# Optimization experiments

Measured on AMD Instinct MI355X. Metric: run time of the kernel, lower is better.

The kernel has to match this reference:

```python
import jax, jax.numpy as jnp
import numpy as np

N_NODES = 50000
N_EDGES = 800000
IN_CH = 128
HID = 128


def setup_inputs() -> dict:
    key = jax.random.key(0)
    ks = jax.random.split(key, 16)
    inp = {
        "x": jax.random.normal(ks[0], (N_NODES, IN_CH), dtype=jnp.float32),
        "edge_index": jax.random.randint(ks[1], (2, N_EDGES), 0, N_NODES, dtype=jnp.int64),
        "batch_size": 1024,
    }
    dims = [(IN_CH, HID), (HID, HID), (HID, HID)]
    for i, (din, dout) in enumerate(dims):
        s = 1.0 / np.sqrt(din)
        inp[f"W_l{i}"] = jax.random.uniform(ks[2 + 4 * i], (dout, din), jnp.float32, -s, s)
        inp[f"b_l{i}"] = jax.random.uniform(ks[3 + 4 * i], (dout,), jnp.float32, -s, s)
        inp[f"W_r{i}"] = jax.random.uniform(ks[4 + 4 * i], (dout, din), jnp.float32, -s, s)
        inp[f"a{i}"] = jnp.full((dout,), 0.25, dtype=jnp.float32)  # PReLU slope
    return inp


def _sage_prelu(x, src, dst, W_l, b_l, W_r, a):
    # mean aggregation of source messages at target nodes
    msg_sum = jax.ops.segment_sum(x[src], dst, num_segments=N_NODES)  # [N, din]
    deg = jax.ops.segment_sum(jnp.ones((src.shape[0],), x.dtype), dst, num_segments=N_NODES)
    agg = msg_sum / jnp.maximum(deg, 1.0)[:, None]
    out = agg @ W_l.T + b_l + x @ W_r.T  # lin_l(aggr) + lin_r(x), bias on lin_l only
    return jnp.where(out > 0, out, a * out)  # per-channel PReLU


def reference(x, edge_index, batch_size, W_l0, b_l0, W_r0, a0, W_l1, b_l1, W_r1, a1, W_l2, b_l2, W_r2, a2):
    src, dst = edge_index[0], edge_index[1]
    x = _sage_prelu(x, src, dst, W_l0, b_l0, W_r0, a0)
    x = _sage_prelu(x, src, dst, W_l1, b_l1, W_r1, a1)
    x = _sage_prelu(x, src, dst, W_l2, b_l2, W_r2, a2)
    return x[:batch_size]
```

## Files before the change

### kernel.cpp

```cpp
#include <hip/hip_runtime.h>

#define NN 50000
#define NE 800000
#define C 128
#define CAP 64
#define EP4 ((NE / 4 + 255) / 256)
#define SPLITB 1563
#define WB 96
#define CB  ((NN + 255) / 256)
#define AGG0B ((NN + 3) / 4)
#define ASTRIDE 136

typedef __attribute__((ext_vector_type(8))) short bf16x8;
typedef __attribute__((ext_vector_type(4))) float f32x4;
typedef unsigned short ushort;

__device__ inline ushort bf16_rn(float f) {
    unsigned u = __builtin_bit_cast(unsigned, f);
    u += 0x7FFF + ((u >> 16) & 1);
    return (ushort)(u >> 16);
}
__device__ inline void split_bf16(float f, ushort& hi, ushort& lo) {
    hi = bf16_rn(f);
    float hif = __builtin_bit_cast(float, (unsigned)hi << 16);
    lo = bf16_rn(f - hif);
}
__device__ inline float bf_lo(unsigned u) { return __builtin_bit_cast(float, u << 16); }
__device__ inline float bf_hi(unsigned u) { return __builtin_bit_cast(float, u & 0xFFFF0000u); }


__global__ __launch_bounds__(256)
void prep_kernel(const int* __restrict__ src, const int* __restrict__ dst,
                 const float* __restrict__ x,
                 const float* __restrict__ W0, const float* __restrict__ W1,
                 const float* __restrict__ W2, const float* __restrict__ W3,
                 const float* __restrict__ W4, const float* __restrict__ W5,
                 int* __restrict__ deg, int* __restrict__ col,
                 ushort* __restrict__ Ah,
                 ushort* __restrict__ Wh, ushort* __restrict__ Wl,
                 int* __restrict__ needed, int rows_out) {
    int t = threadIdx.x;
    if (blockIdx.x < EP4) {
        int e0 = (blockIdx.x * 256 + t) * 4;
        if (e0 < NE) {
            int4 da = *(const int4*)(dst + e0);
            int4 sa = *(const int4*)(src + e0);
            int p0 = atomicAdd(&deg[da.x], 1);
            int p1 = atomicAdd(&deg[da.y], 1);
            int p2 = atomicAdd(&deg[da.z], 1);
            int p3 = atomicAdd(&deg[da.w], 1);
            if (p0 < CAP) col[da.x * CAP + p0] = sa.x;
            if (p1 < CAP) col[da.y * CAP + p1] = sa.y;
            if (p2 < CAP) col[da.z * CAP + p2] = sa.z;
            if (p3 < CAP) col[da.w * CAP + p3] = sa.w;
            if (da.x < rows_out) needed[sa.x] = 1;
            if (da.y < rows_out) needed[sa.y] = 1;
            if (da.z < rows_out) needed[sa.z] = 1;
            if (da.w < rows_out) needed[sa.w] = 1;
        }
    } else if (blockIdx.x < EP4 + SPLITB) {
        int tid = (blockIdx.x - EP4) * 256 + t;
        const int total = NN * C / 4;
        for (int i = tid; i < total; i += SPLITB * 256) {
            f32x4 v = ((const f32x4*)x)[i];
            ushort h0 = bf16_rn(v.x), h1 = bf16_rn(v.y);
            ushort h2 = bf16_rn(v.z), h3 = bf16_rn(v.w);
            *(uint2*)(Ah + (size_t)i * 4) = make_uint2((unsigned)h0 | ((unsigned)h1 << 16),
                                                       (unsigned)h2 | ((unsigned)h3 << 16));
        }
    } else {
        const float* Ws[6] = {W0, W1, W2, W3, W4, W5};
        int i = (blockIdx.x - EP4 - SPLITB) * 256 + t;
        int mat = i >> 12;
        f32x4 v = ((const f32x4*)Ws[mat])[i & 4095];
        ushort h0, h1, h2, h3, l0, l1, l2, l3;
        split_bf16(v.x, h0, l0);
        split_bf16(v.y, h1, l1);
        split_bf16(v.z, h2, l2);
        split_bf16(v.w, h3, l3);
        *(uint2*)(Wh + (size_t)i * 4) = make_uint2((unsigned)h0 | ((unsigned)h1 << 16),
                                                   (unsigned)h2 | ((unsigned)h3 << 16));
        *(uint2*)(Wl + (size_t)i * 4) = make_uint2((unsigned)l0 | ((unsigned)l1 << 16),
                                                   (unsigned)l2 | ((unsigned)l3 << 16));
    }
}


__global__ __launch_bounds__(256)
void agg_kernel(const ushort* __restrict__ xh, const int* __restrict__ deg,
                const int* __restrict__ col,
                const int* __restrict__ list, const int* __restrict__ countp,
                ushort* __restrict__ aggh, ushort* __restrict__ aggl, int nodes,
                int aggblocks, const int* __restrict__ needed,
                int* __restrict__ wlist, int* __restrict__ wcnt, int rows_out) {
    if (needed && blockIdx.x >= aggblocks) {
        int i = (blockIdx.x - aggblocks) * 256 + threadIdx.x;
        if (i < NN && (i < rows_out || needed[i])) {
            int p = atomicAdd(wcnt, 1);
            wlist[p] = i;
        }
        return;
    }
    int i = (blockIdx.x * blockDim.x + threadIdx.x) >> 6;
    int lane = threadIdx.x & 63;
    int cnt = list ? *countp : nodes;
    if (i >= cnt) return;
    int node = list ? list[i] : i;
    int quad = lane >> 4;
    int ql   = lane & 15;
    int d = min(deg[node], CAP);
    int start = node * CAP;
    int end = start + d;
    const uint4* xr = (const uint4*)xh;
    float a0=0,a1=0,a2=0,a3=0,a4=0,a5=0,a6=0,a7=0;
    int e = start;
    for (; e + 15 < end; e += 16) {
        int i0 = col[e + quad];
        int i1 = col[e + 4 + quad];
        int i2 = col[e + 8 + quad];
        int i3 = col[e + 12 + quad];
        uint4 u0 = xr[(size_t)i0 * 16 + ql];
        uint4 u1 = xr[(size_t)i1 * 16 + ql];
        uint4 u2 = xr[(size_t)i2 * 16 + ql];
        uint4 u3 = xr[(size_t)i3 * 16 + ql];
        a0 += (bf_lo(u0.x) + bf_lo(u1.x)) + (bf_lo(u2.x) + bf_lo(u3.x));
        a1 += (bf_hi(u0.x) + bf_hi(u1.x)) + (bf_hi(u2.x) + bf_hi(u3.x));
        a2 += (bf_lo(u0.y) + bf_lo(u1.y)) + (bf_lo(u2.y) + bf_lo(u3.y));
        a3 += (bf_hi(u0.y) + bf_hi(u1.y)) + (bf_hi(u2.y) + bf_hi(u3.y));
        a4 += (bf_lo(u0.z) + bf_lo(u1.z)) + (bf_lo(u2.z) + bf_lo(u3.z));
        a5 += (bf_hi(u0.z) + bf_hi(u1.z)) + (bf_hi(u2.z) + bf_hi(u3.z));
        a6 += (bf_lo(u0.w) + bf_lo(u1.w)) + (bf_lo(u2.w) + bf_lo(u3.w));
        a7 += (bf_hi(u0.w) + bf_hi(u1.w)) + (bf_hi(u2.w) + bf_hi(u3.w));
    }
    for (; e + 7 < end; e += 8) {
        int i0 = col[e + quad];
        int i1 = col[e + 4 + quad];
        uint4 u0 = xr[(size_t)i0 * 16 + ql];
        uint4 u1 = xr[(size_t)i1 * 16 + ql];
        a0 += bf_lo(u0.x) + bf_lo(u1.x); a1 += bf_hi(u0.x) + bf_hi(u1.x);
        a2 += bf_lo(u0.y) + bf_lo(u1.y); a3 += bf_hi(u0.y) + bf_hi(u1.y);
        a4 += bf_lo(u0.z) + bf_lo(u1.z); a5 += bf_hi(u0.z) + bf_hi(u1.z);
        a6 += bf_lo(u0.w) + bf_lo(u1.w); a7 += bf_hi(u0.w) + bf_hi(u1.w);
    }
    for (; e + 3 < end; e += 4) {
        uint4 u = xr[(size_t)col[e + quad] * 16 + ql];
        a0 += bf_lo(u.x); a1 += bf_hi(u.x);
        a2 += bf_lo(u.y); a3 += bf_hi(u.y);
        a4 += bf_lo(u.z); a5 += bf_hi(u.z);
        a6 += bf_lo(u.w); a7 += bf_hi(u.w);
    }
    int rem = end - e;
    if (quad < rem) {
        uint4 u = xr[(size_t)col[e + quad] * 16 + ql];
        a0 += bf_lo(u.x); a1 += bf_hi(u.x);
        a2 += bf_lo(u.y); a3 += bf_hi(u.y);
        a4 += bf_lo(u.z); a5 += bf_hi(u.z);
        a6 += bf_lo(u.w); a7 += bf_hi(u.w);
    }
    a0 += __shfl_xor(a0, 16, 64); a0 += __shfl_xor(a0, 32, 64);
    a1 += __shfl_xor(a1, 16, 64); a1 += __shfl_xor(a1, 32, 64);
    a2 += __shfl_xor(a2, 16, 64); a2 += __shfl_xor(a2, 32, 64);
    a3 += __shfl_xor(a3, 16, 64); a3 += __shfl_xor(a3, 32, 64);
    a4 += __shfl_xor(a4, 16, 64); a4 += __shfl_xor(a4, 32, 64);
    a5 += __shfl_xor(a5, 16, 64); a5 += __shfl_xor(a5, 32, 64);
    a6 += __shfl_xor(a6, 16, 64); a6 += __shfl_xor(a6, 32, 64);
    a7 += __shfl_xor(a7, 16, 64); a7 += __shfl_xor(a7, 32, 64);
    if (quad == 0) {
        float inv = 1.0f / (float)max(d, 1);
        float m[8] = {a0*inv, a1*inv, a2*inv, a3*inv, a4*inv, a5*inv, a6*inv, a7*inv};
        ushort h[8], o[8];
        #pragma unroll
        for (int j = 0; j < 8; ++j) split_bf16(m[j], h[j], o[j]);
        size_t off = (size_t)node * C + ql * 8;
        *(uint4*)(aggh + off) = make_uint4((unsigned)h[0] | ((unsigned)h[1] << 16),
                                           (unsigned)h[2] | ((unsigned)h[3] << 16),
                                           (unsigned)h[4] | ((unsigned)h[5] << 16),
                                           (unsigned)h[6] | ((unsigned)h[7] << 16));
        *(uint4*)(aggl + off) = make_uint4((unsigned)o[0] | ((unsigned)o[1] << 16),
                                           (unsigned)o[2] | ((unsigned)o[3] << 16),
                                           (unsigned)o[4] | ((unsigned)o[5] << 16),
                                           (unsigned)o[6] | ((unsigned)o[7] << 16));
    }
}


__global__ __launch_bounds__(256, 4)
void gemm_kernel(const ushort* __restrict__ Ah, const ushort* __restrict__ Al,
                 const ushort* __restrict__ Xh, const ushort* __restrict__ Xl,
                 const float* __restrict__ Xf,
                 const ushort* __restrict__ Wlh, const ushort* __restrict__ Wll,
                 const ushort* __restrict__ Wrh, const ushort* __restrict__ Wrl,
                 const float* __restrict__ bl, const float* __restrict__ slope,
                 const int* __restrict__ list, const int* __restrict__ countp,
                 float* __restrict__ outf, ushort* __restrict__ outh,
                 ushort* __restrict__ outl, int rows) {
    __shared__ ushort Ahi[64 * ASTRIDE];
    __shared__ ushort Alo[64 * ASTRIDE];
    int t = threadIdx.x;
    int lane = t & 63;
    int w = t >> 6;
    int l = lane & 15;
    int q = lane >> 4;
    int row0 = blockIdx.x * 64;
    int cnt = list ? min(*countp, rows) : rows;
    if (row0 >= cnt) return;

    f32x4 acc[4][2];
    #pragma unroll
    for (int mt = 0; mt < 4; ++mt)
        #pragma unroll
        for (int nt = 0; nt < 2; ++nt)
            acc[mt][nt] = (f32x4){0.f, 0.f, 0.f, 0.f};

    #pragma unroll
    for (int mat = 0; mat < 2; ++mat) {
        const ushort* WH = mat ? Wrh : Wlh;
        const ushort* WL = mat ? Wrl : Wll;
        const ushort* Ph = mat ? Xh : Ah;
        const ushort* Pl = mat ? Xl : Al;

        bf16x8 bhi[2][4], blo[2][4];
        #pragma unroll
        for (int nt = 0; nt < 2; ++nt) {
            int n = w * 32 + nt * 16 + l;
            const ushort* wp = WH + (size_t)n * C + q * 8;
            const ushort* wq = WL + (size_t)n * C + q * 8;
            #pragma unroll
            for (int kb = 0; kb < 4; ++kb) {
                bhi[nt][kb] = *(const bf16x8*)(wp + kb * 32);
                blo[nt][kb] = *(const bf16x8*)(wq + kb * 32);
            }
        }

        __syncthreads();
        int ar = t >> 2;
        int aq = t & 3;
        int ridx = min(row0 + ar, cnt - 1);
        int r = list ? list[ridx] : ridx;
        ushort* dh = Ahi + ar * ASTRIDE + aq * 32;
        ushort* dl = Alo + ar * ASTRIDE + aq * 32;
        if (mat == 1 && Xf) {
            const float* px = Xf + (size_t)r * C + aq * 32;
            #pragma unroll
            for (int i = 0; i < 8; ++i) {
                f32x4 v = *(const f32x4*)(px + i * 4);
                ushort h0, h1, h2, h3, l0, l1, l2, l3;
                split_bf16(v.x, h0, l0);
                split_bf16(v.y, h1, l1);
                split_bf16(v.z, h2, l2);
                split_bf16(v.w, h3, l3);
                *(uint2*)(dh + i * 4) = make_uint2((unsigned)h0 | ((unsigned)h1 << 16),
                                                   (unsigned)h2 | ((unsigned)h3 << 16));
                *(uint2*)(dl + i * 4) = make_uint2((unsigned)l0 | ((unsigned)l1 << 16),
                                                   (unsigned)l2 | ((unsigned)l3 << 16));
            }
        } else {
            const ushort* ph = Ph + (size_t)r * C + aq * 32;
            const ushort* pl = Pl + (size_t)r * C + aq * 32;
            #pragma unroll
            for (int i = 0; i < 4; ++i) {
                *(uint4*)(dh + i * 8) = *(const uint4*)(ph + i * 8);
                *(uint4*)(dl + i * 8) = *(const uint4*)(pl + i * 8);
            }
        }
        __syncthreads();

        #pragma unroll
        for (int kb = 0; kb < 4; ++kb) {
            #pragma unroll
            for (int mt = 0; mt < 4; ++mt) {
                int off = (mt * 16 + l) * ASTRIDE + kb * 32 + q * 8;
                bf16x8 ahi = *(const bf16x8*)(Ahi + off);
                bf16x8 alo = *(const bf16x8*)(Alo + off);
                #pragma unroll
                for (int nt = 0; nt < 2; ++nt) {
                    acc[mt][nt] = __builtin_amdgcn_mfma_f32_16x16x32_bf16(ahi, bhi[nt][kb], acc[mt][nt], 0, 0, 0);
                    acc[mt][nt] = __builtin_amdgcn_mfma_f32_16x16x32_bf16(alo, bhi[nt][kb], acc[mt][nt], 0, 0, 0);
                    acc[mt][nt] = __builtin_amdgcn_mfma_f32_16x16x32_bf16(ahi, blo[nt][kb], acc[mt][nt], 0, 0, 0);
                }
            }
        }
    }

    #pragma unroll
    for (int nt = 0; nt < 2; ++nt) {
        int n = w * 32 + nt * 16 + l;
        float b = bl[n], s = slope[n];
        #pragma unroll
        for (int mt = 0; mt < 4; ++mt) {
            #pragma unroll
            for (int rg = 0; rg < 4; ++rg) {
                int ridx = row0 + mt * 16 + q * 4 + rg;
                if (ridx < cnt) {
                    int r = list ? list[ridx] : ridx;
                    float v = acc[mt][nt][rg] + b;
                    v = v > 0.f ? v : s * v;
                    if (outf) {
                        outf[(size_t)r * C + n] = v;
                    } else {
                        ushort hh, ll;
                        split_bf16(v, hh, ll);
                        outh[(size_t)r * C + n] = hh;
                        outl[(size_t)r * C + n] = ll;
                    }
                }
            }
        }
    }
}


extern "C" void kernel_launch(void* const* d_in, const int* in_sizes, int n_in,
                              void* d_out, int out_size, void* d_ws, size_t ws_size,
                              hipStream_t stream) {
    const float* x   = (const float*)d_in[0];
    const int*   src = (const int*)d_in[1];
    const int*   dst = src + NE;
    const float* Wl[3] = {(const float*)d_in[3], (const float*)d_in[7],  (const float*)d_in[11]};
    const float* bl[3] = {(const float*)d_in[4], (const float*)d_in[8],  (const float*)d_in[12]};
    const float* Wr[3] = {(const float*)d_in[5], (const float*)d_in[9],  (const float*)d_in[13]};
    const float* sl[3] = {(const float*)d_in[6], (const float*)d_in[10], (const float*)d_in[14]};

    int*   deg     = (int*)d_ws;
    int*   needed  = deg + 50016;
    int*   cnt     = needed + 50016;
    int*   col     = cnt + 16;
    int*   list    = col + NN * CAP;
    ushort* Whs    = (ushort*)(list + 50016);
    ushort* Wls    = Whs + 6 * 16384;
    ushort* Gh     = Wls + 6 * 16384;
    ushort* Gl     = Gh + (size_t)NN * C;
    ushort* Ah     = Gl + (size_t)NN * C;
    ushort* Al     = Ah + (size_t)NN * C;
    ushort* Bh     = Al + (size_t)NN * C;
    ushort* Bl     = Bh + (size_t)NN * C;

    int rows_out = out_size / C;

    hipMemsetAsync(deg, 0, (2 * 50016 + 16) * sizeof(int), stream);

    prep_kernel<<<EP4 + SPLITB + WB, 256, 0, stream>>>(
        src, dst, x, Wl[0], Wr[0], Wl[1], Wr[1], Wl[2], Wr[2],
        deg, col, Ah, Whs, Wls, needed, rows_out);

    agg_kernel<<<AGG0B + CB, 256, 0, stream>>>(Ah, deg, col, nullptr, nullptr, Gh, Gl, NN,
                                               AGG0B, needed, list, cnt, rows_out);
    gemm_kernel<<<(NN + 63) / 64, 256, 0, stream>>>(Gh, Gl, nullptr, nullptr, x,
                                                    Whs + 0 * 16384, Wls + 0 * 16384,
                                                    Whs + 1 * 16384, Wls + 1 * 16384,
                                                    bl[0], sl[0], nullptr, nullptr,
                                                    nullptr, Bh, Bl, NN);

    agg_kernel<<<AGG0B, 256, 0, stream>>>(Bh, deg, col, list, cnt, Gh, Gl, NN,
                                          AGG0B, nullptr, nullptr, nullptr, rows_out);
    gemm_kernel<<<(NN + 63) / 64, 256, 0, stream>>>(Gh, Gl, Bh, Bl, nullptr,
                                                    Whs + 2 * 16384, Wls + 2 * 16384,
                                                    Whs + 3 * 16384, Wls + 3 * 16384,
                                                    bl[1], sl[1], list, cnt,
                                                    nullptr, Ah, Al, NN);

    agg_kernel<<<(rows_out + 3) / 4, 256, 0, stream>>>(Ah, deg, col, nullptr, nullptr,
                                                       Gh, Gl, rows_out,
                                                       (rows_out + 3) / 4, nullptr,
                                                       nullptr, nullptr, rows_out);
    gemm_kernel<<<(rows_out + 63) / 64, 256, 0, stream>>>(Gh, Gl, Ah, Al, nullptr,
                                                          Whs + 4 * 16384, Wls + 4 * 16384,
                                                          Whs + 5 * 16384, Wls + 5 * 16384,
                                                          bl[2], sl[2], nullptr, nullptr,
                                                          (float*)d_out, nullptr, nullptr,
                                                          rows_out);
}
```

Measured before the change: 282.9 us.

## Pad degree counters, drop agg low-part, fuse final aggregation with GEMM

```diff
diff --git a/kernel.cpp b/kernel.cpp
--- a/kernel.cpp
+++ b/kernel.cpp
@@ -4,7 +4,8 @@
 #define NE 800000
 #define C 128
 #define CAP 64
-#define EP4 ((NE / 4 + 255) / 256)
+#define DEGS 16
+#define EP16 ((NE / 16 + 255) / 256)
 #define SPLITB 1563
 #define WB 96
 #define CB  ((NN + 255) / 256)
@@ -40,26 +41,29 @@
                  ushort* __restrict__ Wh, ushort* __restrict__ Wl,
                  int* __restrict__ needed, int rows_out) {
     int t = threadIdx.x;
-    if (blockIdx.x < EP4) {
-        int e0 = (blockIdx.x * 256 + t) * 4;
+    if (blockIdx.x < EP16) {
+        int e0 = (blockIdx.x * 256 + t) * 16;
         if (e0 < NE) {
-            int4 da = *(const int4*)(dst + e0);
-            int4 sa = *(const int4*)(src + e0);
-            int p0 = atomicAdd(&deg[da.x], 1);
-            int p1 = atomicAdd(&deg[da.y], 1);
-            int p2 = atomicAdd(&deg[da.z], 1);
-            int p3 = atomicAdd(&deg[da.w], 1);
-            if (p0 < CAP) col[da.x * CAP + p0] = sa.x;
-            if (p1 < CAP) col[da.y * CAP + p1] = sa.y;
-            if (p2 < CAP) col[da.z * CAP + p2] = sa.z;
-            if (p3 < CAP) col[da.w * CAP + p3] = sa.w;
-            if (da.x < rows_out) needed[sa.x] = 1;
-            if (da.y < rows_out) needed[sa.y] = 1;
-            if (da.z < rows_out) needed[sa.z] = 1;
-            if (da.w < rows_out) needed[sa.w] = 1;
-        }
-    } else if (blockIdx.x < EP4 + SPLITB) {
-        int tid = (blockIdx.x - EP4) * 256 + t;
+            #pragma unroll
+            for (int g = 0; g < 4; ++g) {
+                int4 d4 = *(const int4*)(dst + e0 + g * 4);
+                int4 s4 = *(const int4*)(src + e0 + g * 4);
+                int p0 = atomicAdd(&deg[d4.x * DEGS], 1);
+                int p1 = atomicAdd(&deg[d4.y * DEGS], 1);
+                int p2 = atomicAdd(&deg[d4.z * DEGS], 1);
+                int p3 = atomicAdd(&deg[d4.w * DEGS], 1);
+                if (p0 < CAP) col[d4.x * CAP + p0] = s4.x;
+                if (p1 < CAP) col[d4.y * CAP + p1] = s4.y;
+                if (p2 < CAP) col[d4.z * CAP + p2] = s4.z;
+                if (p3 < CAP) col[d4.w * CAP + p3] = s4.w;
+                if (d4.x < rows_out) needed[s4.x] = 1;
+                if (d4.y < rows_out) needed[s4.y] = 1;
+                if (d4.z < rows_out) needed[s4.z] = 1;
+                if (d4.w < rows_out) needed[s4.w] = 1;
+            }
+        }
+    } else if (blockIdx.x < EP16 + SPLITB) {
+        int tid = (blockIdx.x - EP16) * 256 + t;
         const int total = NN * C / 4;
         for (int i = tid; i < total; i += SPLITB * 256) {
             f32x4 v = ((const f32x4*)x)[i];
@@ -70,7 +74,7 @@
         }
     } else {
         const float* Ws[6] = {W0, W1, W2, W3, W4, W5};
-        int i = (blockIdx.x - EP4 - SPLITB) * 256 + t;
+        int i = (blockIdx.x - EP16 - SPLITB) * 256 + t;
         int mat = i >> 12;
         f32x4 v = ((const f32x4*)Ws[mat])[i & 4095];
         ushort h0, h1, h2, h3, l0, l1, l2, l3;
@@ -90,7 +94,7 @@
 void agg_kernel(const ushort* __restrict__ xh, const int* __restrict__ deg,
                 const int* __restrict__ col,
                 const int* __restrict__ list, const int* __restrict__ countp,
-                ushort* __restrict__ aggh, ushort* __restrict__ aggl, int nodes,
+                ushort* __restrict__ aggh, int nodes,
                 int aggblocks, const int* __restrict__ needed,
                 int* __restrict__ wlist, int* __restrict__ wcnt, int rows_out) {
     if (needed && blockIdx.x >= aggblocks) {
@@ -108,7 +112,7 @@
     int node = list ? list[i] : i;
     int quad = lane >> 4;
     int ql   = lane & 15;
-    int d = min(deg[node], CAP);
+    int d = min(deg[node * DEGS], CAP);
     int start = node * CAP;
     int end = start + d;
     const uint4* xr = (const uint4*)xh;
@@ -168,24 +172,20 @@
     if (quad == 0) {
         float inv = 1.0f / (float)max(d, 1);
         float m[8] = {a0*inv, a1*inv, a2*inv, a3*inv, a4*inv, a5*inv, a6*inv, a7*inv};
-        ushort h[8], o[8];
-        #pragma unroll
-        for (int j = 0; j < 8; ++j) split_bf16(m[j], h[j], o[j]);
+        ushort h[8];
+        #pragma unroll
+        for (int j = 0; j < 8; ++j) h[j] = bf16_rn(m[j]);
         size_t off = (size_t)node * C + ql * 8;
         *(uint4*)(aggh + off) = make_uint4((unsigned)h[0] | ((unsigned)h[1] << 16),
                                            (unsigned)h[2] | ((unsigned)h[3] << 16),
                                            (unsigned)h[4] | ((unsigned)h[5] << 16),
                                            (unsigned)h[6] | ((unsigned)h[7] << 16));
-        *(uint4*)(aggl + off) = make_uint4((unsigned)o[0] | ((unsigned)o[1] << 16),
-                                           (unsigned)o[2] | ((unsigned)o[3] << 16),
-                                           (unsigned)o[4] | ((unsigned)o[5] << 16),
-                                           (unsigned)o[6] | ((unsigned)o[7] << 16));
     }
 }
 
 
 __global__ __launch_bounds__(256, 4)
-void gemm_kernel(const ushort* __restrict__ Ah, const ushort* __restrict__ Al,
+void gemm_kernel(const ushort* __restrict__ Ag,
                  const ushort* __restrict__ Xh, const ushort* __restrict__ Xl,
                  const float* __restrict__ Xf,
                  const ushort* __restrict__ Wlh, const ushort* __restrict__ Wll,
@@ -216,8 +216,6 @@
     for (int mat = 0; mat < 2; ++mat) {
         const ushort* WH = mat ? Wrh : Wlh;
         const ushort* WL = mat ? Wrl : Wll;
-        const ushort* Ph = mat ? Xh : Ah;
-        const ushort* Pl = mat ? Xl : Al;
 
         bf16x8 bhi[2][4], blo[2][4];
         #pragma unroll
@@ -239,7 +237,12 @@
         int r = list ? list[ridx] : ridx;
         ushort* dh = Ahi + ar * ASTRIDE + aq * 32;
         ushort* dl = Alo + ar * ASTRIDE + aq * 32;
-        if (mat == 1 && Xf) {
+        if (mat == 0) {
+            const ushort* ph = Ag + (size_t)r * C + aq * 32;
+            #pragma unroll
+            for (int i = 0; i < 4; ++i)
+                *(uint4*)(dh + i * 8) = *(const uint4*)(ph + i * 8);
+        } else if (Xf) {
             const float* px = Xf + (size_t)r * C + aq * 32;
             #pragma unroll
             for (int i = 0; i < 8; ++i) {
@@ -255,8 +258,8 @@
                                                    (unsigned)l2 | ((unsigned)l3 << 16));
             }
         } else {
-            const ushort* ph = Ph + (size_t)r * C + aq * 32;
-            const ushort* pl = Pl + (size_t)r * C + aq * 32;
+            const ushort* ph = Xh + (size_t)r * C + aq * 32;
+            const ushort* pl = Xl + (size_t)r * C + aq * 32;
             #pragma unroll
             for (int i = 0; i < 4; ++i) {
                 *(uint4*)(dh + i * 8) = *(const uint4*)(ph + i * 8);
@@ -271,11 +274,13 @@
             for (int mt = 0; mt < 4; ++mt) {
                 int off = (mt * 16 + l) * ASTRIDE + kb * 32 + q * 8;
                 bf16x8 ahi = *(const bf16x8*)(Ahi + off);
-                bf16x8 alo = *(const bf16x8*)(Alo + off);
                 #pragma unroll
                 for (int nt = 0; nt < 2; ++nt) {
                     acc[mt][nt] = __builtin_amdgcn_mfma_f32_16x16x32_bf16(ahi, bhi[nt][kb], acc[mt][nt], 0, 0, 0);
-                    acc[mt][nt] = __builtin_amdgcn_mfma_f32_16x16x32_bf16(alo, bhi[nt][kb], acc[mt][nt], 0, 0, 0);
+                    if (mat == 1) {
+                        bf16x8 alo = *(const bf16x8*)(Alo + off);
+                        acc[mt][nt] = __builtin_amdgcn_mfma_f32_16x16x32_bf16(alo, bhi[nt][kb], acc[mt][nt], 0, 0, 0);
+                    }
                     acc[mt][nt] = __builtin_amdgcn_mfma_f32_16x16x32_bf16(ahi, blo[nt][kb], acc[mt][nt], 0, 0, 0);
                 }
             }
@@ -310,6 +315,151 @@
 }
 
 
+__global__ __launch_bounds__(256)
+void fused_kernel(const ushort* __restrict__ Gsrc,
+                  const int* __restrict__ deg, const int* __restrict__ col,
+                  const ushort* __restrict__ Xh, const ushort* __restrict__ Xl,
+                  const ushort* __restrict__ Wlh, const ushort* __restrict__ Wll,
+                  const ushort* __restrict__ Wrh, const ushort* __restrict__ Wrl,
+                  const float* __restrict__ bl, const float* __restrict__ slope,
+                  float* __restrict__ outf, int rows) {
+    __shared__ ushort Ahi[64 * ASTRIDE];
+    __shared__ ushort Alo[64 * ASTRIDE];
+    int t = threadIdx.x;
+    int lane = t & 63;
+    int w = t >> 6;
+    int l = lane & 15;
+    int q = lane >> 4;
+    int row0 = blockIdx.x * 64;
+    if (row0 >= rows) return;
+
+    f32x4 acc[4][2];
+    #pragma unroll
+    for (int mt = 0; mt < 4; ++mt)
+        #pragma unroll
+        for (int nt = 0; nt < 2; ++nt)
+            acc[mt][nt] = (f32x4){0.f, 0.f, 0.f, 0.f};
+
+    #pragma unroll
+    for (int mat = 0; mat < 2; ++mat) {
+        const ushort* WH = mat ? Wrh : Wlh;
+        const ushort* WL = mat ? Wrl : Wll;
+
+        bf16x8 bhi[2][4], blo[2][4];
+        #pragma unroll
+        for (int nt = 0; nt < 2; ++nt) {
+            int n = w * 32 + nt * 16 + l;
+            const ushort* wp = WH + (size_t)n * C + q * 8;
+            const ushort* wq = WL + (size_t)n * C + q * 8;
+            #pragma unroll
+            for (int kb = 0; kb < 4; ++kb) {
+                bhi[nt][kb] = *(const bf16x8*)(wp + kb * 32);
+                blo[nt][kb] = *(const bf16x8*)(wq + kb * 32);
+            }
+        }
+
+        __syncthreads();
+        int ar = t >> 2;
+        int aq = t & 3;
+        int r = min(row0 + ar, rows - 1);
+        ushort* dh = Ahi + ar * ASTRIDE + aq * 32;
+        ushort* dl = Alo + ar * ASTRIDE + aq * 32;
+        if (mat == 0) {
+            int d = min(deg[r * DEGS], CAP);
+            int base = r * CAP;
+            float s[32];
+            #pragma unroll
+            for (int j = 0; j < 32; ++j) s[j] = 0.f;
+#define ACC8(k, u, v) \
+            s[(k)+0] += bf_lo((u).x) + bf_lo((v).x); s[(k)+1] += bf_hi((u).x) + bf_hi((v).x); \
+            s[(k)+2] += bf_lo((u).y) + bf_lo((v).y); s[(k)+3] += bf_hi((u).y) + bf_hi((v).y); \
+            s[(k)+4] += bf_lo((u).z) + bf_lo((v).z); s[(k)+5] += bf_hi((u).z) + bf_hi((v).z); \
+            s[(k)+6] += bf_lo((u).w) + bf_lo((v).w); s[(k)+7] += bf_hi((u).w) + bf_hi((v).w);
+#define ACC8S(k, u) \
+            s[(k)+0] += bf_lo((u).x); s[(k)+1] += bf_hi((u).x); \
+            s[(k)+2] += bf_lo((u).y); s[(k)+3] += bf_hi((u).y); \
+            s[(k)+4] += bf_lo((u).z); s[(k)+5] += bf_hi((u).z); \
+            s[(k)+6] += bf_lo((u).w); s[(k)+7] += bf_hi((u).w);
+            int e = 0;
+            for (; e + 1 < d; e += 2) {
+                int2 c01 = *(const int2*)(col + base + e);
+                const uint4* p0 = (const uint4*)Gsrc + (size_t)c01.x * 16 + aq * 4;
+                const uint4* p1 = (const uint4*)Gsrc + (size_t)c01.y * 16 + aq * 4;
+                uint4 a0 = p0[0], a1 = p0[1], a2 = p0[2], a3 = p0[3];
+                uint4 b0 = p1[0], b1 = p1[1], b2 = p1[2], b3 = p1[3];
+                ACC8(0, a0, b0) ACC8(8, a1, b1) ACC8(16, a2, b2) ACC8(24, a3, b3)
+            }
+            if (e < d) {
+                int c0 = col[base + e];
+                const uint4* p0 = (const uint4*)Gsrc + (size_t)c0 * 16 + aq * 4;
+                uint4 a0 = p0[0], a1 = p0[1], a2 = p0[2], a3 = p0[3];
+                ACC8S(0, a0) ACC8S(8, a1) ACC8S(16, a2) ACC8S(24, a3)
+            }
+#undef ACC8
+#undef ACC8S
+            float inv = 1.0f / (float)max(d, 1);
+            #pragma unroll
+            for (int i = 0; i < 4; ++i) {
+                ushort h[8], o[8];
+                #pragma unroll
+                for (int j = 0; j < 8; ++j) split_bf16(s[i * 8 + j] * inv, h[j], o[j]);
+                *(uint4*)(dh + i * 8) = make_uint4((unsigned)h[0] | ((unsigned)h[1] << 16),
+                                                   (unsigned)h[2] | ((unsigned)h[3] << 16),
+                                                   (unsigned)h[4] | ((unsigned)h[5] << 16),
+                                                   (unsigned)h[6] | ((unsigned)h[7] << 16));
+                *(uint4*)(dl + i * 8) = make_uint4((unsigned)o[0] | ((unsigned)o[1] << 16),
+                                                   (unsigned)o[2] | ((unsigned)o[3] << 16),
+                                                   (unsigned)o[4] | ((unsigned)o[5] << 16),
+                                                   (unsigned)o[6] | ((unsigned)o[7] << 16));
+            }
+        } else {
+            const ushort* ph = Xh + (size_t)r * C + aq * 32;
+            const ushort* pl = Xl + (size_t)r * C + aq * 32;
+            #pragma unroll
+            for (int i = 0; i < 4; ++i) {
+                *(uint4*)(dh + i * 8) = *(const uint4*)(ph + i * 8);
+                *(uint4*)(dl + i * 8) = *(const uint4*)(pl + i * 8);
+            }
+        }
+        __syncthreads();
+
+        #pragma unroll
+        for (int kb = 0; kb < 4; ++kb) {
+            #pragma unroll
+            for (int mt = 0; mt < 4; ++mt) {
+                int off = (mt * 16 + l) * ASTRIDE + kb * 32 + q * 8;
+                bf16x8 ahi = *(const bf16x8*)(Ahi + off);
+                bf16x8 alo = *(const bf16x8*)(Alo + off);
+                #pragma unroll
+                for (int nt = 0; nt < 2; ++nt) {
+                    acc[mt][nt] = __builtin_amdgcn_mfma_f32_16x16x32_bf16(ahi, bhi[nt][kb], acc[mt][nt], 0, 0, 0);
+                    acc[mt][nt] = __builtin_amdgcn_mfma_f32_16x16x32_bf16(alo, bhi[nt][kb], acc[mt][nt], 0, 0, 0);
+                    acc[mt][nt] = __builtin_amdgcn_mfma_f32_16x16x32_bf16(ahi, blo[nt][kb], acc[mt][nt], 0, 0, 0);
+                }
+            }
+        }
+    }
+
+    #pragma unroll
+    for (int nt = 0; nt < 2; ++nt) {
+        int n = w * 32 + nt * 16 + l;
+        float b = bl[n], s = slope[n];
+        #pragma unroll
+        for (int mt = 0; mt < 4; ++mt) {
+            #pragma unroll
+            for (int rg = 0; rg < 4; ++rg) {
+                int ridx = row0 + mt * 16 + q * 4 + rg;
+                if (ridx < rows) {
+                    float v = acc[mt][nt][rg] + b;
+                    v = v > 0.f ? v : s * v;
+                    outf[(size_t)ridx * C + n] = v;
+                }
+            }
+        }
+    }
+}
+
+
 extern "C" void kernel_launch(void* const* d_in, const int* in_sizes, int n_in,
                               void* d_out, int out_size, void* d_ws, size_t ws_size,
                               hipStream_t stream) {
@@ -322,51 +472,45 @@
     const float* sl[3] = {(const float*)d_in[6], (const float*)d_in[10], (const float*)d_in[14]};
 
     int*   deg     = (int*)d_ws;
-    int*   needed  = deg + 50016;
+    int*   needed  = deg + NN * DEGS;
     int*   cnt     = needed + 50016;
     int*   col     = cnt + 16;
     int*   list    = col + NN * CAP;
     ushort* Whs    = (ushort*)(list + 50016);
     ushort* Wls    = Whs + 6 * 16384;
     ushort* Gh     = Wls + 6 * 16384;
-    ushort* Gl     = Gh + (size_t)NN * C;
-    ushort* Ah     = Gl + (size_t)NN * C;
+    ushort* Ah     = Gh + (size_t)NN * C;
     ushort* Al     = Ah + (size_t)NN * C;
     ushort* Bh     = Al + (size_t)NN * C;
     ushort* Bl     = Bh + (size_t)NN * C;
 
     int rows_out = out_size / C;
 
-    hipMemsetAsync(deg, 0, (2 * 50016 + 16) * sizeof(int), stream);
-
-    prep_kernel<<<EP4 + SPLITB + WB, 256, 0, stream>>>(
+    hipMemsetAsync(deg, 0, (NN * DEGS + 50016 + 16) * sizeof(int), stream);
+
+    prep_kernel<<<EP16 + SPLITB + WB, 256, 0, stream>>>(
         src, dst, x, Wl[0], Wr[0], Wl[1], Wr[1], Wl[2], Wr[2],
         deg, col, Ah, Whs, Wls, needed, rows_out);
 
-    agg_kernel<<<AGG0B + CB, 256, 0, stream>>>(Ah, deg, col, nullptr, nullptr, Gh, Gl, NN,
+    agg_kernel<<<AGG0B + CB, 256, 0, stream>>>(Ah, deg, col, nullptr, nullptr, Gh, NN,
                                                AGG0B, needed, list, cnt, rows_out);
-    gemm_kernel<<<(NN + 63) / 64, 256, 0, stream>>>(Gh, Gl, nullptr, nullptr, x,
+    gemm_kernel<<<(NN + 63) / 64, 256, 0, stream>>>(Gh, nullptr, nullptr, x,
                                                     Whs + 0 * 16384, Wls + 0 * 16384,
                                                     Whs + 1 * 16384, Wls + 1 * 16384,
                                                     bl[0], sl[0], nullptr, nullptr,
                                                     nullptr, Bh, Bl, NN);
 
-    agg_kernel<<<AGG0B, 256, 0, stream>>>(Bh, deg, col, list, cnt, Gh, Gl, NN,
+    agg_kernel<<<AGG0B, 256, 0, stream>>>(Bh, deg, col, list, cnt, Gh, NN,
                                           AGG0B, nullptr, nullptr, nullptr, rows_out);
-    gemm_kernel<<<(NN + 63) / 64, 256, 0, stream>>>(Gh, Gl, Bh, Bl, nullptr,
+    gemm_kernel<<<(NN + 63) / 64, 256, 0, stream>>>(Gh, Bh, Bl, nullptr,
                                                     Whs + 2 * 16384, Wls + 2 * 16384,
                                                     Whs + 3 * 16384, Wls + 3 * 16384,
                                                     bl[1], sl[1], list, cnt,
                                                     nullptr, Ah, Al, NN);
 
-    agg_kernel<<<(rows_out + 3) / 4, 256, 0, stream>>>(Ah, deg, col, nullptr, nullptr,
-                                                       Gh, Gl, rows_out,
-                                                       (rows_out + 3) / 4, nullptr,
-                                                       nullptr, nullptr, rows_out);
-    gemm_kernel<<<(rows_out + 63) / 64, 256, 0, stream>>>(Gh, Gl, Ah, Al, nullptr,
-                                                          Whs + 4 * 16384, Wls + 4 * 16384,
-                                                          Whs + 5 * 16384, Wls + 5 * 16384,
-                                                          bl[2], sl[2], nullptr, nullptr,
-                                                          (float*)d_out, nullptr, nullptr,
-                                                          rows_out);
-}
+    fused_kernel<<<(rows_out + 63) / 64, 256, 0, stream>>>(Ah, deg, col, Ah, Al,
+                                                           Whs + 4 * 16384, Wls + 4 * 16384,
+                                                           Whs + 5 * 16384, Wls + 5 * 16384,
+                                                           bl[2], sl[2],
+                                                           (float*)d_out, rows_out);
+}
```

After: 272.9 us. -3.5%, faster.
